# Optimization experiments

Hardware: AMD Instinct MI355X
Metric: run time of the kernel (lower is better)

The kernel has to match this reference:

```python
import jax, jax.numpy as jnp
import numpy as np

N = 2_000_000   # points
C = 65_536      # cluster centers
F = 8           # point feature dim
D = 3           # coord dim


def _dense_params(key, din, dout):
    kw, kb = jax.random.split(key)
    scale = jnp.sqrt(2.0 / din).astype(jnp.float32)
    return (jax.random.normal(kw, (din, dout), jnp.float32) * scale,
            jnp.zeros((dout,), jnp.float32))


def setup_inputs() -> dict:
    key = jax.random.key(0)
    ks = jax.random.split(key, 16)
    inp = {
        "point_features": jax.random.normal(ks[0], (N, F), jnp.float32),
        "labels": jax.random.randint(ks[1], (N,), 0, C, jnp.int32),
        "cluster_centers": jax.random.normal(ks[2], (C, D), jnp.float32),
        "points": jax.random.normal(ks[3], (N, D), jnp.float32),
    }
    # edge MLP: (F+D)->8->16->32->64
    dims = [F + D, 8, 16, 32, 64]
    for i in range(4):
        w, b = _dense_params(ks[4 + i], dims[i], dims[i + 1])
        inp[f"we{i}"] = w
        inp[f"be{i}"] = b
    # attention MLP: (F+D)->64->1
    inp["wa0"], inp["ba0"] = _dense_params(ks[8], F + D, 64)
    inp["wa1"], inp["ba1"] = _dense_params(ks[9], 64, 1)
    # output MLP: 64->128->256
    inp["wo0"], inp["bo0"] = _dense_params(ks[10], 64, 128)
    inp["wo1"], inp["bo1"] = _dense_params(ks[11], 128, 256)
    return inp


def reference(point_features, labels, cluster_centers, points,
              we0, be0, we1, be1, we2, be2, we3, be3,
              wa0, ba0, wa1, ba1, wo0, bo0, wo1, bo1):
    relu = jax.nn.relu
    # gather center coords for each point, build edge input [N, F+D]
    center_coords = cluster_centers[labels]
    x = jnp.concatenate([point_features, center_coords - points], axis=-1)
    # edge MLP 8->16->32->64 (all relu)
    h = relu(x @ we0 + be0)
    h = relu(h @ we1 + be1)
    h = relu(h @ we2 + be2)
    h = relu(h @ we3 + be3)            # [N, 64]
    # attention MLP 64->1 sigmoid
    a = relu(x @ wa0 + ba0)
    a = jax.nn.sigmoid(a @ wa1 + ba1)  # [N, 1]
    t = h * a
    # scatter-sum into clusters
    agg = jax.ops.segment_sum(t, labels, num_segments=C)  # [C, 64]
    # output MLP 128->256 (relu, relu)
    o = relu(agg @ wo0 + bo0)
    o = relu(o @ wo1 + bo1)            # [C, 256]
    return o
```

## Files before the change

kernel.cpp:

```cpp
#include <hip/hip_runtime.h>
#include <hip/hip_bf16.h>
#include <math.h>
#include <stdint.h>

#define TPB 256
#define NCB 32
#define SAGG_LD 68
#define SMID_LD 132

typedef float f32x4 __attribute__((ext_vector_type(4)));
typedef short bf16x8 __attribute__((ext_vector_type(8)));

__device__ inline unsigned int bf16bits(float f)
{
    __hip_bfloat16 b = __float2bfloat16(f);
    return (unsigned int)(*(unsigned short*)&b);
}

__device__ inline unsigned int bfpack(float lo, float hi)
{
    return bf16bits(lo) | (bf16bits(hi) << 16);
}

__global__ __launch_bounds__(TPB) void hist_kernel(
    const int* __restrict__ labels, int* __restrict__ counts, int n)
{
    int i = blockIdx.x * TPB + threadIdx.x;
    if (i < n) atomicAdd(&counts[labels[i]], 1);
}

__global__ __launch_bounds__(256) void scan_local(
    const int* __restrict__ counts, int* __restrict__ off,
    int* __restrict__ bsum, int C)
{
    __shared__ int sh[256];
    int t = threadIdx.x;
    int i = blockIdx.x * 256 + t;
    int v = (i < C) ? counts[i] : 0;
    sh[t] = v;
    __syncthreads();
    for (int d = 1; d < 256; d <<= 1) {
        int u = (t >= d) ? sh[t - d] : 0;
        __syncthreads();
        sh[t] += u;
        __syncthreads();
    }
    if (i < C) off[i] = sh[t] - v;
    if (t == 255) bsum[blockIdx.x] = sh[255];
}

__global__ __launch_bounds__(256) void scan_base(
    int* __restrict__ bsum, int* __restrict__ off, int nb, int C)
{
    __shared__ int sh[256];
    int t = threadIdx.x;
    int v = (t < nb) ? bsum[t] : 0;
    sh[t] = v;
    __syncthreads();
    for (int d = 1; d < 256; d <<= 1) {
        int u = (t >= d) ? sh[t - d] : 0;
        __syncthreads();
        sh[t] += u;
        __syncthreads();
    }
    if (t < nb) bsum[t] = sh[t] - v;
    if (t == 255) off[C] = sh[255];
}

__global__ __launch_bounds__(256) void scan_apply(
    int* __restrict__ off, int* __restrict__ cursor,
    const int* __restrict__ bsum, int C)
{
    int i = blockIdx.x * 256 + threadIdx.x;
    if (i < C) {
        int v = off[i] + bsum[blockIdx.x];
        off[i] = v;
        cursor[i] = v;
    }
}

__global__ __launch_bounds__(TPB, 4) void point_mlp_kernel(
    const float* __restrict__ pf, const int* __restrict__ labels,
    const float* __restrict__ centers, const float* __restrict__ points,
    const float* __restrict__ we0, const float* __restrict__ be0,
    const float* __restrict__ we1, const float* __restrict__ be1,
    const float* __restrict__ we2, const float* __restrict__ be2,
    const float* __restrict__ we3, const float* __restrict__ be3,
    const float* __restrict__ wa0, const float* __restrict__ ba0,
    const float* __restrict__ wa1, const float* __restrict__ ba1,
    int* __restrict__ cursor, unsigned short* __restrict__ tsort, int n)
{
    __shared__ unsigned int s_stage[4][32][64];

    int tid  = threadIdx.x;
    int lane = tid & 63;
    int w    = tid >> 6;
    int lg   = lane >> 4;
    int lm   = lane & 15;
    int pbase = blockIdx.x * TPB + w * 64;

    int i0 = blockIdx.x * TPB + tid;
    int i  = (i0 < n) ? i0 : (n - 1);

    float x[11];
    const float4* pf4 = (const float4*)pf;
    float4 p0 = pf4[(size_t)i * 2 + 0];
    float4 p1 = pf4[(size_t)i * 2 + 1];
    x[0] = p0.x; x[1] = p0.y; x[2] = p0.z; x[3] = p0.w;
    x[4] = p1.x; x[5] = p1.y; x[6] = p1.z; x[7] = p1.w;

    int lbl = labels[i];
    x[8]  = centers[lbl * 3 + 0] - points[(size_t)i * 3 + 0];
    x[9]  = centers[lbl * 3 + 1] - points[(size_t)i * 3 + 1];
    x[10] = centers[lbl * 3 + 2] - points[(size_t)i * 3 + 2];

    int pos = 0;
    if (i0 < n) pos = atomicAdd(&cursor[lbl], 1);

#pragma unroll
    for (int r = 0; r < 16; r++) {
        unsigned int v = 0;
        if (2 * r < 11)     v  = bf16bits(x[2 * r]);
        if (2 * r + 1 < 11) v |= bf16bits(x[2 * r + 1]) << 16;
        s_stage[w][r][lane] = v;
    }

    float h1[8];
#pragma unroll
    for (int j = 0; j < 8; j++) {
        float v = be0[j];
#pragma unroll
        for (int k = 0; k < 11; k++) v = fmaf(x[k], we0[k * 8 + j], v);
        h1[j] = fmaxf(v, 0.f);
    }
    float h2[16];
#pragma unroll
    for (int j = 0; j < 16; j++) {
        float v = be1[j];
#pragma unroll
        for (int k = 0; k < 8; k++) v = fmaf(h1[k], we1[k * 16 + j], v);
        h2[j] = fmaxf(v, 0.f);
    }

    bf16x8 a_at[4];
#pragma unroll
    for (int mt = 0; mt < 4; mt++) {
        union { unsigned int u[4]; bf16x8 v; } au;
#pragma unroll
        for (int ii = 0; ii < 4; ii++) {
            int k0 = lg * 8 + 2 * ii;
            int j  = mt * 16 + lm;
            unsigned int u = 0;
            if (k0 < 11)     u  = bf16bits(wa0[k0 * 64 + j]);
            if (k0 + 1 < 11) u |= bf16bits(wa0[(k0 + 1) * 64 + j]) << 16;
            au.u[ii] = u;
        }
        a_at[mt] = au.v;
    }

    float gate_arr[4];
#pragma unroll
    for (int nt = 0; nt < 4; nt++) {
        int spt = nt * 16 + lm;
        union { unsigned int u[4]; bf16x8 v; } bu;
#pragma unroll
        for (int ii = 0; ii < 4; ii++) bu.u[ii] = s_stage[w][lg * 4 + ii][spt];

        float part = 0.f;
#pragma unroll
        for (int mt = 0; mt < 4; mt++) {
            f32x4 acc = {0.f, 0.f, 0.f, 0.f};
            acc = __builtin_amdgcn_mfma_f32_16x16x32_bf16(a_at[mt], bu.v, acc, 0, 0, 0);
            int jb = mt * 16 + lg * 4;
            const float4 b0 = *(const float4*)&ba0[jb];
            const float4 w1 = *(const float4*)&wa1[jb];
            part = fmaf(fmaxf(acc[0] + b0.x, 0.f), w1.x, part);
            part = fmaf(fmaxf(acc[1] + b0.y, 0.f), w1.y, part);
            part = fmaf(fmaxf(acc[2] + b0.z, 0.f), w1.z, part);
            part = fmaf(fmaxf(acc[3] + b0.w, 0.f), w1.w, part);
        }
        part += __shfl_xor(part, 16, 64);
        part += __shfl_xor(part, 32, 64);
        float s = ba1[0] + part;
        gate_arr[nt] = 1.f / (1.f + __expf(-s));
    }

#pragma unroll
    for (int r = 0; r < 8; r++)
        s_stage[w][r][lane] = bfpack(h2[2 * r], h2[2 * r + 1]);

    bf16x8 a_l2[2];
#pragma unroll
    for (int mt = 0; mt < 2; mt++) {
        union { unsigned int u[4]; bf16x8 v; } au;
#pragma unroll
        for (int ii = 0; ii < 4; ii++) {
            int k0 = lg * 8 + 2 * ii;
            int j  = mt * 16 + lm;
            unsigned int u = 0;
            if (k0 < 16)     u  = bf16bits(we2[k0 * 32 + j]);
            if (k0 + 1 < 16) u |= bf16bits(we2[(k0 + 1) * 32 + j]) << 16;
            au.u[ii] = u;
        }
        a_l2[mt] = au.v;
    }

#pragma unroll
    for (int nt = 0; nt < 4; nt++) {
        int spt = nt * 16 + lm;
        union { unsigned int u[4]; bf16x8 v; } bu;
#pragma unroll
        for (int ii = 0; ii < 4; ii++) bu.u[ii] = s_stage[w][lg * 4 + ii][spt];

#pragma unroll
        for (int mt = 0; mt < 2; mt++) {
            f32x4 acc = {0.f, 0.f, 0.f, 0.f};
            acc = __builtin_amdgcn_mfma_f32_16x16x32_bf16(a_l2[mt], bu.v, acc, 0, 0, 0);
            const float4 b2 = *(const float4*)&be2[mt * 16 + lg * 4];
            float d0 = fmaxf(acc[0] + b2.x, 0.f);
            float d1 = fmaxf(acc[1] + b2.y, 0.f);
            float d2 = fmaxf(acc[2] + b2.z, 0.f);
            float d3 = fmaxf(acc[3] + b2.w, 0.f);
            s_stage[w][16 + mt * 8 + lg * 2 + 0][spt] = bfpack(d0, d1);
            s_stage[w][16 + mt * 8 + lg * 2 + 1][spt] = bfpack(d2, d3);
        }
    }

    bf16x8 a_l3[4];
#pragma unroll
    for (int mt = 0; mt < 4; mt++) {
        union { unsigned int u[4]; bf16x8 v; } au;
#pragma unroll
        for (int ii = 0; ii < 4; ii++) {
            int k0 = lg * 8 + 2 * ii;
            int j  = mt * 16 + lm;
            au.u[ii] = bfpack(we3[k0 * 64 + j], we3[(k0 + 1) * 64 + j]);
        }
        a_l3[mt] = au.v;
    }

#pragma unroll
    for (int nt = 0; nt < 4; nt++) {
        int   spt   = nt * 16 + lm;
        float g     = gate_arr[nt];
        int   ppos  = __shfl(pos, spt, 64);
        bool  valid = (pbase + spt) < n;

        union { unsigned int u[4]; bf16x8 v; } bu;
#pragma unroll
        for (int ii = 0; ii < 4; ii++) bu.u[ii] = s_stage[w][16 + lg * 4 + ii][spt];

#pragma unroll
        for (int mt = 0; mt < 4; mt++) {
            f32x4 acc = {0.f, 0.f, 0.f, 0.f};
            acc = __builtin_amdgcn_mfma_f32_16x16x32_bf16(a_l3[mt], bu.v, acc, 0, 0, 0);
            int jb = mt * 16 + lg * 4;
            const float4 bias = *(const float4*)&be3[jb];
            float v0 = fmaxf(acc[0] + bias.x, 0.f) * g;
            float v1 = fmaxf(acc[1] + bias.y, 0.f) * g;
            float v2 = fmaxf(acc[2] + bias.z, 0.f) * g;
            float v3 = fmaxf(acc[3] + bias.w, 0.f) * g;
            if (valid) {
                unsigned int d0 = bfpack(v0, v1);
                unsigned int d1 = bfpack(v2, v3);
                *(uint2*)((unsigned int*)tsort + (size_t)ppos * 32 + (jb >> 1)) =
                    make_uint2(d0, d1);
            }
        }
    }
}

__global__ __launch_bounds__(TPB) void agg_outmlp_kernel(
    const unsigned short* __restrict__ tsort,
    const int* __restrict__ off,
    const float* __restrict__ wo0, const float* __restrict__ bo0,
    const float* __restrict__ wo1, const float* __restrict__ bo1,
    float* __restrict__ out)
{
    __shared__ float s_agg[NCB * SAGG_LD];
    __shared__ float s_mid[NCB * SMID_LD];
    int tid = threadIdx.x;
    int c0 = blockIdx.x * NCB;

    {
        int lane  = tid & 63;
        int w     = tid >> 6;
        int rlane = lane >> 3;
        int word  = lane & 7;
        const uint4* t128 = (const uint4*)tsort;
#define BF_LO(u) (__uint_as_float((u) << 16))
#define BF_HI(u) (__uint_as_float((u) & 0xffff0000u))
        for (int lc = w * 8; lc < w * 8 + 8; lc++) {
            int rb = off[c0 + lc];
            int re = off[c0 + lc + 1];
            float a[8];
#pragma unroll
            for (int q = 0; q < 8; q++) a[q] = 0.f;
            for (int r = rb; r < re; r += 16) {
                int r0 = r + rlane;
                int r1 = r + 8 + rlane;
                uint4 v0 = make_uint4(0u, 0u, 0u, 0u);
                uint4 v1 = make_uint4(0u, 0u, 0u, 0u);
                if (r0 < re) v0 = t128[(size_t)r0 * 8 + word];
                if (r1 < re) v1 = t128[(size_t)r1 * 8 + word];
                a[0] += BF_LO(v0.x) + BF_LO(v1.x);
                a[1] += BF_HI(v0.x) + BF_HI(v1.x);
                a[2] += BF_LO(v0.y) + BF_LO(v1.y);
                a[3] += BF_HI(v0.y) + BF_HI(v1.y);
                a[4] += BF_LO(v0.z) + BF_LO(v1.z);
                a[5] += BF_HI(v0.z) + BF_HI(v1.z);
                a[6] += BF_LO(v0.w) + BF_LO(v1.w);
                a[7] += BF_HI(v0.w) + BF_HI(v1.w);
            }
#pragma unroll
            for (int m = 8; m < 64; m <<= 1) {
#pragma unroll
                for (int q = 0; q < 8; q++) a[q] += __shfl_xor(a[q], m, 64);
            }
            if (rlane == 0) {
                *(float4*)&s_agg[lc * SAGG_LD + word * 8 + 0] =
                    make_float4(a[0], a[1], a[2], a[3]);
                *(float4*)&s_agg[lc * SAGG_LD + word * 8 + 4] =
                    make_float4(a[4], a[5], a[6], a[7]);
            }
        }
#undef BF_LO
#undef BF_HI
    }
    __syncthreads();

    {
        int mg = tid & 15;
        int cg = tid >> 4;
        int m0 = mg * 8;
        float acc[2][8];
#pragma unroll
        for (int mi = 0; mi < 8; mi++) {
            float b = bo0[m0 + mi];
            acc[0][mi] = b;
            acc[1][mi] = b;
        }
        for (int k = 0; k < 64; k += 4) {
            float4 a0 = *(const float4*)&s_agg[(cg * 2 + 0) * SAGG_LD + k];
            float4 a1 = *(const float4*)&s_agg[(cg * 2 + 1) * SAGG_LD + k];
            float av0[4] = {a0.x, a0.y, a0.z, a0.w};
            float av1[4] = {a1.x, a1.y, a1.z, a1.w};
#pragma unroll
            for (int q = 0; q < 4; q++) {
                float4 wlo = *(const float4*)&wo0[(k + q) * 128 + m0];
                float4 whi = *(const float4*)&wo0[(k + q) * 128 + m0 + 4];
                float wv[8] = {wlo.x, wlo.y, wlo.z, wlo.w,
                               whi.x, whi.y, whi.z, whi.w};
#pragma unroll
                for (int mi = 0; mi < 8; mi++) {
                    acc[0][mi] = fmaf(av0[q], wv[mi], acc[0][mi]);
                    acc[1][mi] = fmaf(av1[q], wv[mi], acc[1][mi]);
                }
            }
        }
#pragma unroll
        for (int c = 0; c < 2; c++) {
            float4 lo = make_float4(fmaxf(acc[c][0], 0.f), fmaxf(acc[c][1], 0.f),
                                    fmaxf(acc[c][2], 0.f), fmaxf(acc[c][3], 0.f));
            float4 hi = make_float4(fmaxf(acc[c][4], 0.f), fmaxf(acc[c][5], 0.f),
                                    fmaxf(acc[c][6], 0.f), fmaxf(acc[c][7], 0.f));
            *(float4*)&s_mid[(cg * 2 + c) * SMID_LD + m0 + 0] = lo;
            *(float4*)&s_mid[(cg * 2 + c) * SMID_LD + m0 + 4] = hi;
        }
    }
    __syncthreads();

    {
        int mg = tid & 31;
        int cg = tid >> 5;
        int m0 = mg * 8;
        float acc[4][8];
#pragma unroll
        for (int mi = 0; mi < 8; mi++) {
            float b = bo1[m0 + mi];
            acc[0][mi] = b;
            acc[1][mi] = b;
            acc[2][mi] = b;
            acc[3][mi] = b;
        }
        for (int j = 0; j < 128; j += 4) {
            float4 a0 = *(const float4*)&s_mid[(cg * 4 + 0) * SMID_LD + j];
            float4 a1 = *(const float4*)&s_mid[(cg * 4 + 1) * SMID_LD + j];
            float4 a2 = *(const float4*)&s_mid[(cg * 4 + 2) * SMID_LD + j];
            float4 a3 = *(const float4*)&s_mid[(cg * 4 + 3) * SMID_LD + j];
            float av0[4] = {a0.x, a0.y, a0.z, a0.w};
            float av1[4] = {a1.x, a1.y, a1.z, a1.w};
            float av2[4] = {a2.x, a2.y, a2.z, a2.w};
            float av3[4] = {a3.x, a3.y, a3.z, a3.w};
#pragma unroll
            for (int q = 0; q < 4; q++) {
                float4 wlo = *(const float4*)&wo1[(j + q) * 256 + m0];
                float4 whi = *(const float4*)&wo1[(j + q) * 256 + m0 + 4];
                float wv[8] = {wlo.x, wlo.y, wlo.z, wlo.w,
                               whi.x, whi.y, whi.z, whi.w};
#pragma unroll
                for (int mi = 0; mi < 8; mi++) {
                    acc[0][mi] = fmaf(av0[q], wv[mi], acc[0][mi]);
                    acc[1][mi] = fmaf(av1[q], wv[mi], acc[1][mi]);
                    acc[2][mi] = fmaf(av2[q], wv[mi], acc[2][mi]);
                    acc[3][mi] = fmaf(av3[q], wv[mi], acc[3][mi]);
                }
            }
        }
#pragma unroll
        for (int c = 0; c < 4; c++) {
            float4 lo = make_float4(fmaxf(acc[c][0], 0.f), fmaxf(acc[c][1], 0.f),
                                    fmaxf(acc[c][2], 0.f), fmaxf(acc[c][3], 0.f));
            float4 hi = make_float4(fmaxf(acc[c][4], 0.f), fmaxf(acc[c][5], 0.f),
                                    fmaxf(acc[c][6], 0.f), fmaxf(acc[c][7], 0.f));
            size_t row = (size_t)(c0 + cg * 4 + c) * 256 + m0;
            *(float4*)&out[row + 0] = lo;
            *(float4*)&out[row + 4] = hi;
        }
    }
}

extern "C" void kernel_launch(void* const* d_in, const int* in_sizes, int n_in,
                              void* d_out, int out_size, void* d_ws, size_t ws_size,
                              hipStream_t stream)
{
    const float* pf      = (const float*)d_in[0];
    const int*   labels  = (const int*)d_in[1];
    const float* centers = (const float*)d_in[2];
    const float* points  = (const float*)d_in[3];
    const float* we0 = (const float*)d_in[4];
    const float* be0 = (const float*)d_in[5];
    const float* we1 = (const float*)d_in[6];
    const float* be1 = (const float*)d_in[7];
    const float* we2 = (const float*)d_in[8];
    const float* be2 = (const float*)d_in[9];
    const float* we3 = (const float*)d_in[10];
    const float* be3 = (const float*)d_in[11];
    const float* wa0 = (const float*)d_in[12];
    const float* ba0 = (const float*)d_in[13];
    const float* wa1 = (const float*)d_in[14];
    const float* ba1 = (const float*)d_in[15];
    const float* wo0 = (const float*)d_in[16];
    const float* bo0 = (const float*)d_in[17];
    const float* wo1 = (const float*)d_in[18];
    const float* bo1 = (const float*)d_in[19];
    float* out = (float*)d_out;

    int n = in_sizes[0] / 8;
    int C = in_sizes[2] / 3;

    int* counts = (int*)d_ws;
    int* cursor = counts + C;
    int* off    = cursor + C;
    int* bsum   = off + C + 1;
    uintptr_t tb = ((uintptr_t)(bsum + 256) + 255) & ~(uintptr_t)255;
    unsigned short* tsort = (unsigned short*)tb;

    hipMemsetAsync(counts, 0, (size_t)C * sizeof(int), stream);

    int pblocks = (n + TPB - 1) / TPB;
    int nb = (C + 255) / 256;
    hist_kernel<<<pblocks, TPB, 0, stream>>>(labels, counts, n);
    scan_local<<<nb, 256, 0, stream>>>(counts, off, bsum, C);
    scan_base<<<1, 256, 0, stream>>>(bsum, off, nb, C);
    scan_apply<<<nb, 256, 0, stream>>>(off, cursor, bsum, C);

    point_mlp_kernel<<<pblocks, TPB, 0, stream>>>(
        pf, labels, centers, points,
        we0, be0, we1, be1, we2, be2, we3, be3,
        wa0, ba0, wa1, ba1, cursor, tsort, n);

    agg_outmlp_kernel<<<C / NCB, TPB, 0, stream>>>(
        tsort, off, wo0, bo0, wo1, bo1, out);
}
```

Before: 595.7 us.

## Compute attention gate with scalar FMAs and halve shared staging buffer

The attention MLP (11->64->1) now runs as per-thread fp32 FMA loops instead of bf16 MFMA tiles, which removes the x staging writes and the gate shuffle reduction. The shared staging buffer is halved by reusing rows for h2 and h3, with all layer-2 operands loaded up front and layer-3 inputs held in registers before write-back. Sched barriers pin the ordering of these phases. The scalar gate path adds about 700 FMAs per point and more weight loads, traded against lower LDS use, fewer LDS round trips and likely higher occupancy.

```diff
diff --git a/kernel.cpp b/kernel.cpp
--- a/kernel.cpp
+++ b/kernel.cpp
@@ -90,7 +90,7 @@
     const float* __restrict__ wa1, const float* __restrict__ ba1,
     int* __restrict__ cursor, unsigned short* __restrict__ tsort, int n)
 {
-    __shared__ unsigned int s_stage[4][32][64];
+    __shared__ unsigned int s_stage[4][16][64];
 
     int tid  = threadIdx.x;
     int lane = tid & 63;
@@ -117,13 +117,16 @@
     int pos = 0;
     if (i0 < n) pos = atomicAdd(&cursor[lbl], 1);
 
-#pragma unroll
-    for (int r = 0; r < 16; r++) {
-        unsigned int v = 0;
-        if (2 * r < 11)     v  = bf16bits(x[2 * r]);
-        if (2 * r + 1 < 11) v |= bf16bits(x[2 * r + 1]) << 16;
-        s_stage[w][r][lane] = v;
-    }
+    float s = ba1[0];
+#pragma unroll
+    for (int j = 0; j < 64; j++) {
+        float aj = ba0[j];
+#pragma unroll
+        for (int k = 0; k < 11; k++) aj = fmaf(x[k], wa0[k * 64 + j], aj);
+        aj = fmaxf(aj, 0.f);
+        s = fmaf(aj, wa1[j], s);
+    }
+    float gate = 1.f / (1.f + __expf(-s));
 
     float h1[8];
 #pragma unroll
@@ -142,52 +145,12 @@
         h2[j] = fmaxf(v, 0.f);
     }
 
-    bf16x8 a_at[4];
-#pragma unroll
-    for (int mt = 0; mt < 4; mt++) {
-        union { unsigned int u[4]; bf16x8 v; } au;
-#pragma unroll
-        for (int ii = 0; ii < 4; ii++) {
-            int k0 = lg * 8 + 2 * ii;
-            int j  = mt * 16 + lm;
-            unsigned int u = 0;
-            if (k0 < 11)     u  = bf16bits(wa0[k0 * 64 + j]);
-            if (k0 + 1 < 11) u |= bf16bits(wa0[(k0 + 1) * 64 + j]) << 16;
-            au.u[ii] = u;
-        }
-        a_at[mt] = au.v;
-    }
-
-    float gate_arr[4];
-#pragma unroll
-    for (int nt = 0; nt < 4; nt++) {
-        int spt = nt * 16 + lm;
-        union { unsigned int u[4]; bf16x8 v; } bu;
-#pragma unroll
-        for (int ii = 0; ii < 4; ii++) bu.u[ii] = s_stage[w][lg * 4 + ii][spt];
-
-        float part = 0.f;
-#pragma unroll
-        for (int mt = 0; mt < 4; mt++) {
-            f32x4 acc = {0.f, 0.f, 0.f, 0.f};
-            acc = __builtin_amdgcn_mfma_f32_16x16x32_bf16(a_at[mt], bu.v, acc, 0, 0, 0);
-            int jb = mt * 16 + lg * 4;
-            const float4 b0 = *(const float4*)&ba0[jb];
-            const float4 w1 = *(const float4*)&wa1[jb];
-            part = fmaf(fmaxf(acc[0] + b0.x, 0.f), w1.x, part);
-            part = fmaf(fmaxf(acc[1] + b0.y, 0.f), w1.y, part);
-            part = fmaf(fmaxf(acc[2] + b0.z, 0.f), w1.z, part);
-            part = fmaf(fmaxf(acc[3] + b0.w, 0.f), w1.w, part);
-        }
-        part += __shfl_xor(part, 16, 64);
-        part += __shfl_xor(part, 32, 64);
-        float s = ba1[0] + part;
-        gate_arr[nt] = 1.f / (1.f + __expf(-s));
-    }
-
 #pragma unroll
     for (int r = 0; r < 8; r++)
         s_stage[w][r][lane] = bfpack(h2[2 * r], h2[2 * r + 1]);
+#pragma unroll
+    for (int r = 8; r < 16; r++)
+        s_stage[w][r][lane] = 0u;
 
     bf16x8 a_l2[2];
 #pragma unroll
@@ -205,13 +168,34 @@
         a_l2[mt] = au.v;
     }
 
+    bf16x8 a_l3[4];
+#pragma unroll
+    for (int mt = 0; mt < 4; mt++) {
+        union { unsigned int u[4]; bf16x8 v; } au;
+#pragma unroll
+        for (int ii = 0; ii < 4; ii++) {
+            int k0 = lg * 8 + 2 * ii;
+            int j  = mt * 16 + lm;
+            au.u[ii] = bfpack(we3[k0 * 64 + j], we3[(k0 + 1) * 64 + j]);
+        }
+        a_l3[mt] = au.v;
+    }
+
+    unsigned int bu_all[4][4];
 #pragma unroll
     for (int nt = 0; nt < 4; nt++) {
-        int spt = nt * 16 + lm;
+#pragma unroll
+        for (int ii = 0; ii < 4; ii++)
+            bu_all[nt][ii] = s_stage[w][lg * 4 + ii][nt * 16 + lm];
+    }
+    __builtin_amdgcn_sched_barrier(0);
+
+    unsigned int h3w[4][2][2];
+#pragma unroll
+    for (int nt = 0; nt < 4; nt++) {
         union { unsigned int u[4]; bf16x8 v; } bu;
 #pragma unroll
-        for (int ii = 0; ii < 4; ii++) bu.u[ii] = s_stage[w][lg * 4 + ii][spt];
-
+        for (int ii = 0; ii < 4; ii++) bu.u[ii] = bu_all[nt][ii];
 #pragma unroll
         for (int mt = 0; mt < 2; mt++) {
             f32x4 acc = {0.f, 0.f, 0.f, 0.f};
@@ -221,34 +205,31 @@
             float d1 = fmaxf(acc[1] + b2.y, 0.f);
             float d2 = fmaxf(acc[2] + b2.z, 0.f);
             float d3 = fmaxf(acc[3] + b2.w, 0.f);
-            s_stage[w][16 + mt * 8 + lg * 2 + 0][spt] = bfpack(d0, d1);
-            s_stage[w][16 + mt * 8 + lg * 2 + 1][spt] = bfpack(d2, d3);
-        }
-    }
-
-    bf16x8 a_l3[4];
-#pragma unroll
-    for (int mt = 0; mt < 4; mt++) {
-        union { unsigned int u[4]; bf16x8 v; } au;
-#pragma unroll
-        for (int ii = 0; ii < 4; ii++) {
-            int k0 = lg * 8 + 2 * ii;
-            int j  = mt * 16 + lm;
-            au.u[ii] = bfpack(we3[k0 * 64 + j], we3[(k0 + 1) * 64 + j]);
-        }
-        a_l3[mt] = au.v;
-    }
+            h3w[nt][mt][0] = bfpack(d0, d1);
+            h3w[nt][mt][1] = bfpack(d2, d3);
+        }
+    }
+
+#pragma unroll
+    for (int nt = 0; nt < 4; nt++) {
+#pragma unroll
+        for (int mt = 0; mt < 2; mt++) {
+            s_stage[w][mt * 8 + lg * 2 + 0][nt * 16 + lm] = h3w[nt][mt][0];
+            s_stage[w][mt * 8 + lg * 2 + 1][nt * 16 + lm] = h3w[nt][mt][1];
+        }
+    }
+    __builtin_amdgcn_sched_barrier(0);
 
 #pragma unroll
     for (int nt = 0; nt < 4; nt++) {
         int   spt   = nt * 16 + lm;
-        float g     = gate_arr[nt];
-        int   ppos  = __shfl(pos, spt, 64);
+        float g     = __shfl(gate, spt, 64);
+        int   ppos  = __shfl(pos,  spt, 64);
         bool  valid = (pbase + spt) < n;
 
         union { unsigned int u[4]; bf16x8 v; } bu;
 #pragma unroll
-        for (int ii = 0; ii < 4; ii++) bu.u[ii] = s_stage[w][16 + lg * 4 + ii][spt];
+        for (int ii = 0; ii < 4; ii++) bu.u[ii] = s_stage[w][lg * 4 + ii][spt];
 
 #pragma unroll
         for (int mt = 0; mt < 4; mt++) {
```

New measurement: 603.2 us. No clear change (+1.3%).
